# Performance work log

Measured on AMD Instinct MI355X. Metric: run time of the kernel, lower is better.

Reference implementation:

```python
import jax, jax.numpy as jnp
import numpy as np

N_NODES = 50000
IN_CH = 256
OUT_CH = 128
HID = 2 * OUT_CH  # 256
N_EDGES = 800000


def setup_inputs() -> dict:
    key = jax.random.key(0)
    ks = jax.random.split(key, 12)
    glorot = lambda k, shape: jax.random.normal(k, shape, jnp.float32) * (2.0 / sum(shape)) ** 0.5
    return {
        "x": jax.random.normal(ks[0], (N_NODES, IN_CH), jnp.float32),
        "edge_index": jax.random.randint(ks[1], (2, N_EDGES), 0, N_NODES),
        "conv_w": glorot(ks[2], (IN_CH, HID)),      # MetaGCNConv weight: x @ W
        "conv_b": jnp.zeros((HID,), jnp.float32),
        "fc1_w": glorot(ks[3], (HID, HID)), "fc1_b": jnp.zeros((HID,), jnp.float32),
        "fc2_w": glorot(ks[4], (HID, HID)), "fc2_b": jnp.zeros((HID,), jnp.float32),
        "fc3_w": glorot(ks[5], (OUT_CH, HID)), "fc3_b": jnp.zeros((OUT_CH,), jnp.float32),
        "fc4_w": glorot(ks[6], (OUT_CH, HID)), "fc4_b": jnp.zeros((OUT_CH,), jnp.float32),
    }


def reference(x, edge_index, conv_w, conv_b, fc1_w, fc1_b, fc2_w, fc2_b, fc3_w, fc3_b, fc4_w, fc4_b):
    N = x.shape[0]
    # GCN with added self-loops and symmetric normalization (PyG GCNConv semantics)
    loop = jnp.arange(N)
    src = jnp.concatenate([edge_index[0], loop])
    dst = jnp.concatenate([edge_index[1], loop])
    xw = x @ conv_w  # [N, HID]
    ones = jnp.ones_like(src, dtype=x.dtype)
    deg = jax.ops.segment_sum(ones, src, num_segments=N)
    dinv = jnp.where(deg > 0, jax.lax.rsqrt(deg), 0.0)
    norm = dinv[src] * dinv[dst]  # [E+N]
    agg = jax.ops.segment_sum(norm[:, None] * xw[src], dst, num_segments=N)  # [N, HID]
    h = jax.nn.relu(agg + conv_b)
    s = h.sum(0)  # [HID]
    lin = lambda v, w, b: jnp.tanh(v @ w.T + b)
    return (lin(s, fc1_w, fc1_b), lin(s, fc2_w, fc2_b), lin(s, fc3_w, fc3_b), lin(s, fc4_w, fc4_b))
```

## Files before the change

kernel.cpp:

```cpp
#include <hip/hip_runtime.h>
#include <math.h>

#define CH 256
#define BCAP 64

typedef short bf16x8 __attribute__((ext_vector_type(8)));
typedef float f32x4 __attribute__((ext_vector_type(4)));
typedef unsigned int u32;

__device__ __forceinline__ unsigned short f2bf(float f) {
    u32 u = __float_as_uint(f);
    u += 0x7FFFu + ((u >> 16) & 1u);
    return (unsigned short)(u >> 16);
}
__device__ __forceinline__ float bf2f(unsigned short h) {
    return __uint_as_float(((u32)h) << 16);
}
__device__ __forceinline__ float lo16f(u32 q) { return __uint_as_float(q << 16); }
__device__ __forceinline__ float hi16f(u32 q) { return __uint_as_float(q & 0xffff0000u); }
__device__ __forceinline__ u32 pkbf(float a, float b) {
    u32 ua = __float_as_uint(a) + 0x8000u;
    u32 ub = __float_as_uint(b) + 0x8000u;
    return __builtin_amdgcn_perm(ub, ua, 0x07060302u);
}
__device__ __forceinline__ void async16(const void* g, void* l) {
    __builtin_amdgcn_global_load_lds((const __attribute__((address_space(1))) u32*)g,
                                     (__attribute__((address_space(3))) u32*)l, 16, 0, 0);
}

__global__ __launch_bounds__(256) void prep_kernel(const float* __restrict__ W,
                                                   unsigned short* __restrict__ whiT,
                                                   unsigned short* __restrict__ wloT,
                                                   float4* __restrict__ zbase,
                                                   int zcount4) {
    int b = blockIdx.x, t = threadIdx.x;
    if (b < 64) {
#pragma unroll
        for (int i = 0; i < 4; i++) {
            int n = b * 4 + i;
            float w = W[(size_t)t * CH + n];
            unsigned short hi = f2bf(w);
            unsigned short lo = f2bf(w - bf2f(hi));
            whiT[(size_t)n * CH + t] = hi;
            wloT[(size_t)n * CH + t] = lo;
        }
    } else {
        int i = (b - 64) * 256 + t;
        int stride = 104 * 256;
        float4 z = make_float4(0.f, 0.f, 0.f, 0.f);
        for (; i < zcount4; i += stride) zbase[i] = z;
    }
}

__global__ __launch_bounds__(256) void mega_kernel(const float* __restrict__ x,
                                                   const unsigned short* __restrict__ whiT,
                                                   const unsigned short* __restrict__ wloT,
                                                   const int* __restrict__ ei,
                                                   unsigned* __restrict__ cnt_src,
                                                   unsigned* __restrict__ cnt_dst,
                                                   unsigned* __restrict__ col,
                                                   unsigned short* __restrict__ y,
                                                   int M, int E, int G) {
    int b = blockIdx.x, t = threadIdx.x;
    if (b < 2 * G && !(b & 1)) {
        __shared__ __align__(16) unsigned short smA [128 * 32];
        __shared__ __align__(16) unsigned short smBh[128 * 32];
        __shared__ __align__(16) unsigned short smBl[128 * 32];
        int g = b >> 1;
        int lane = t & 63, w = t >> 6;
        int m0 = (g >> 1) * 128;
        int n0 = (g & 1) * 128;
        int mo = (w >> 1) * 64, no = (w & 1) * 64;
        int quad = lane >> 4, l16 = lane & 15;

        f32x4 acc[4][4] = {};

        int arow = t >> 1, ahalf = t & 1;
        int gm = min(m0 + arow, M - 1);
        const float* xrow = x + (size_t)gm * CH + ahalf * 16;
        int idx0 = t, idx1 = t + 256;
        size_t gb0 = (size_t)(n0 + (idx0 >> 2)) * CH + (idx0 & 3) * 8;
        size_t gb1 = (size_t)(n0 + (idx1 >> 2)) * CH + (idx1 & 3) * 8;

        for (int k0 = 0; k0 < CH; k0 += 32) {
            const float4* xp = (const float4*)(xrow + k0);
            float4 v0 = xp[0], v1 = xp[1], v2 = xp[2], v3 = xp[3];
            async16(&whiT[gb0 + k0], &smBh[idx0 * 8]);
            async16(&whiT[gb1 + k0], &smBh[idx1 * 8]);
            async16(&wloT[gb0 + k0], &smBl[idx0 * 8]);
            async16(&wloT[gb1 + k0], &smBl[idx1 * 8]);
            uint4 w0 = make_uint4(pkbf(v0.x, v0.y), pkbf(v0.z, v0.w),
                                  pkbf(v1.x, v1.y), pkbf(v1.z, v1.w));
            uint4 w1 = make_uint4(pkbf(v2.x, v2.y), pkbf(v2.z, v2.w),
                                  pkbf(v3.x, v3.y), pkbf(v3.z, v3.w));
            *(uint4*)&smA[arow * 32 + ahalf * 16]     = w0;
            *(uint4*)&smA[arow * 32 + ahalf * 16 + 8] = w1;
            __syncthreads();

            bf16x8 a[4], bh[4], bl[4];
#pragma unroll
            for (int i = 0; i < 4; i++)
                a[i] = *(const bf16x8*)&smA[(mo + i * 16 + l16) * 32 + quad * 8];
#pragma unroll
            for (int j = 0; j < 4; j++) {
                bh[j] = *(const bf16x8*)&smBh[(no + j * 16 + l16) * 32 + quad * 8];
                bl[j] = *(const bf16x8*)&smBl[(no + j * 16 + l16) * 32 + quad * 8];
            }
#pragma unroll
            for (int i = 0; i < 4; i++)
#pragma unroll
                for (int j = 0; j < 4; j++) {
                    acc[i][j] = __builtin_amdgcn_mfma_f32_16x16x32_bf16(a[i], bh[j], acc[i][j], 0, 0, 0);
                    acc[i][j] = __builtin_amdgcn_mfma_f32_16x16x32_bf16(a[i], bl[j], acc[i][j], 0, 0, 0);
                }
            __syncthreads();
        }
#pragma unroll
        for (int i = 0; i < 4; i++) {
            int mbase = m0 + mo + i * 16 + quad * 4;
#pragma unroll
            for (int r = 0; r < 4; r++) {
                int m = mbase + r;
                if (m < M) {
#pragma unroll
                    for (int j = 0; j < 4; j++) {
                        int ncol = n0 + no + j * 16 + l16;
                        int s = ncol >> 5, c = ncol & 31;
                        y[((size_t)s * M + m) * 32 + c] = f2bf(acc[i][j][r]);
                    }
                }
            }
        }
    } else {
        int fb = (b < 2 * G) ? (b >> 1) : (b - G);
        if (fb >= 1024) return;
        int i = fb * 256 + t;
        int stride = 1024 * 256;
        for (; i < E; i += stride) {
            int s = ei[i];
            int d = ei[E + i];
            atomicAdd(&cnt_src[s], 1u);
            unsigned pos = atomicAdd(&cnt_dst[d], 1u);
            if (pos < BCAP) col[(size_t)d * BCAP + pos] = (unsigned)s;
        }
    }
}

__global__ __launch_bounds__(256) void scale_kernel(unsigned short* __restrict__ y,
                                                    const unsigned* __restrict__ cnt_src,
                                                    int M) {
    int gid = blockIdx.x * 256 + threadIdx.x;
    int gstride = gridDim.x * 256;
    int total4 = M * 4;
    uint4* yq = (uint4*)y;
    for (int s = 0; s < 8; s++) {
        for (int c = gid; c < total4; c += gstride) {
            int m = c >> 2;
            float dv = rsqrtf((float)(cnt_src[m] + 1u));
            uint4 q = yq[(size_t)s * total4 + c];
            q.x = pkbf(dv * lo16f(q.x), dv * hi16f(q.x));
            q.y = pkbf(dv * lo16f(q.y), dv * hi16f(q.y));
            q.z = pkbf(dv * lo16f(q.z), dv * hi16f(q.z));
            q.w = pkbf(dv * lo16f(q.w), dv * hi16f(q.w));
            yq[(size_t)s * total4 + c] = q;
        }
    }
}

__global__ __launch_bounds__(256) void gather_kernel(const unsigned short* __restrict__ y,
                                                     const unsigned* __restrict__ cnt_src,
                                                     const unsigned* __restrict__ cnt_dst,
                                                     const unsigned* __restrict__ col,
                                                     const float* __restrict__ bias,
                                                     float* __restrict__ s_sum, int N) {
    int t = threadIdx.x;
    int lane = t & 63, wv = t >> 6;
    int slice = blockIdx.x & 7;
    int grp   = blockIdx.x >> 3;
    int ng = lane >> 4;
    int g  = (lane >> 2) & 3;
    int li = lane & 3;
    const unsigned short* ys = y + (size_t)slice * N * 32;

    float b8[8];
#pragma unroll
    for (int j = 0; j < 8; j++) b8[j] = bias[slice * 32 + li * 8 + j];

    float ts[8] = {0.f, 0.f, 0.f, 0.f, 0.f, 0.f, 0.f, 0.f};

    int wid = grp * 4 + wv;
    int nw  = (gridDim.x >> 3) * 4;

    for (int base = wid * 4; base < N; base += nw * 4) {
        int n = min(base + ng, N - 1);
        unsigned deg = min(cnt_dst[n], (unsigned)BCAP);
        unsigned cnt = deg + 1;
        float gnm = (g == 0 && base + ng < N) ? 1.f : 0.f;
        unsigned mc = cnt;
        mc = max(mc, (unsigned)__shfl_xor((int)mc, 16, 64));
        mc = max(mc, (unsigned)__shfl_xor((int)mc, 32, 64));

        const unsigned* cb = col + (size_t)n * BCAP;
        float acc[8] = {0.f, 0.f, 0.f, 0.f, 0.f, 0.f, 0.f, 0.f};
        for (unsigned k = 0; k < mc; k += 4) {
            unsigned r = k + g;
            unsigned src = (r < deg) ? cb[r] : (unsigned)n;
            float m = (r < cnt) ? 1.f : 0.f;
            uint4 q = *(const uint4*)(ys + (size_t)src * 32 + li * 8);
            acc[0] = fmaf(m, lo16f(q.x), acc[0]);
            acc[1] = fmaf(m, hi16f(q.x), acc[1]);
            acc[2] = fmaf(m, lo16f(q.y), acc[2]);
            acc[3] = fmaf(m, hi16f(q.y), acc[3]);
            acc[4] = fmaf(m, lo16f(q.z), acc[4]);
            acc[5] = fmaf(m, hi16f(q.z), acc[5]);
            acc[6] = fmaf(m, lo16f(q.w), acc[6]);
            acc[7] = fmaf(m, hi16f(q.w), acc[7]);
        }
        float dv = rsqrtf((float)(cnt_src[n] + 1u));
#pragma unroll
        for (int j = 0; j < 8; j++) {
            float v = acc[j];
            v += __shfl_xor(v, 4, 64);
            v += __shfl_xor(v, 8, 64);
            float h = fmaxf(fmaf(dv, v, b8[j]), 0.f);
            ts[j] = fmaf(gnm, h, ts[j]);
        }
    }

#pragma unroll
    for (int j = 0; j < 8; j++) {
        float v = ts[j];
        v += __shfl_xor(v, 16, 64);
        v += __shfl_xor(v, 32, 64);
        ts[j] = v;
    }

    __shared__ float red[4][32];
    if (lane < 4) {
#pragma unroll
        for (int j = 0; j < 8; j++) red[wv][lane * 8 + j] = ts[j];
    }
    __syncthreads();
    if (t < 32) {
        atomicAdd(&s_sum[slice * 32 + t],
                  red[0][t] + red[1][t] + red[2][t] + red[3][t]);
    }
}

__global__ __launch_bounds__(256) void fc_kernel(const float* __restrict__ s_sum,
                                                 const float* __restrict__ fc1_w, const float* __restrict__ fc1_b,
                                                 const float* __restrict__ fc2_w, const float* __restrict__ fc2_b,
                                                 const float* __restrict__ fc3_w, const float* __restrict__ fc3_b,
                                                 const float* __restrict__ fc4_w, const float* __restrict__ fc4_b,
                                                 float* __restrict__ out) {
    int wid  = (blockIdx.x * blockDim.x + threadIdx.x) >> 6;
    int lane = threadIdx.x & 63;
    if (wid >= 768) return;
    const float* w; const float* b; int row, obase;
    if (wid < 256)      { w = fc1_w; b = fc1_b; row = wid;       obase = 0;   }
    else if (wid < 512) { w = fc2_w; b = fc2_b; row = wid - 256; obase = 256; }
    else if (wid < 640) { w = fc3_w; b = fc3_b; row = wid - 512; obase = 512; }
    else                { w = fc4_w; b = fc4_b; row = wid - 640; obase = 640; }
    float4 wv = *(const float4*)&w[(size_t)row * 256 + lane * 4];
    float4 sv = *(const float4*)&s_sum[lane * 4];
    float d = wv.x * sv.x + wv.y * sv.y + wv.z * sv.z + wv.w * sv.w;
#pragma unroll
    for (int off = 32; off; off >>= 1) d += __shfl_down(d, off, 64);
    if (lane == 0) out[obase + row] = tanhf(d + b[row]);
}

extern "C" void kernel_launch(void* const* d_in, const int* in_sizes, int n_in,
                              void* d_out, int out_size, void* d_ws, size_t ws_size,
                              hipStream_t stream) {
    const float* x      = (const float*)d_in[0];
    const int*   ei     = (const int*)d_in[1];
    const float* conv_w = (const float*)d_in[2];
    const float* conv_b = (const float*)d_in[3];
    const float* fc1_w  = (const float*)d_in[4];
    const float* fc1_b  = (const float*)d_in[5];
    const float* fc2_w  = (const float*)d_in[6];
    const float* fc2_b  = (const float*)d_in[7];
    const float* fc3_w  = (const float*)d_in[8];
    const float* fc3_b  = (const float*)d_in[9];
    const float* fc4_w  = (const float*)d_in[10];
    const float* fc4_b  = (const float*)d_in[11];
    float* out = (float*)d_out;

    const int N = in_sizes[0] / CH;
    const int E = in_sizes[1] / 2;
    const int G = ((N + 127) / 128) * 2;

    char* ws = (char*)d_ws;
    size_t off = 0;
    auto alloc = [&](size_t bytes) -> void* {
        off = (off + 255) & ~(size_t)255;
        void* p = ws + off;
        off += bytes;
        return p;
    };
    unsigned* cnt_src = (unsigned*)alloc((size_t)N * 4);
    unsigned* cnt_dst = (unsigned*)alloc((size_t)N * 4);
    float*    s_sum   = (float*)alloc((size_t)CH * 4);
    size_t zero_bytes = off;
    unsigned* col     = (unsigned*)alloc((size_t)N * BCAP * 4);
    unsigned short* whiT = (unsigned short*)alloc((size_t)CH * CH * 2);
    unsigned short* wloT = (unsigned short*)alloc((size_t)CH * CH * 2);
    unsigned short* y    = (unsigned short*)alloc((size_t)N * CH * 2);

    int zcount4 = (int)((zero_bytes + 15) / 16);

    prep_kernel<<<168, 256, 0, stream>>>(conv_w, whiT, wloT, (float4*)ws, zcount4);
    mega_kernel<<<G + 1024, 256, 0, stream>>>(x, whiT, wloT, ei,
                                              cnt_src, cnt_dst, col, y, N, E, G);
    scale_kernel<<<1024, 256, 0, stream>>>(y, cnt_src, N);
    gather_kernel<<<2048, 256, 0, stream>>>(y, cnt_src, cnt_dst, col, conv_b, s_sum, N);
    fc_kernel<<<192, 256, 0, stream>>>(s_sum,
                                       fc1_w, fc1_b, fc2_w, fc2_b,
                                       fc3_w, fc3_b, fc4_w, fc4_b, out);
}
```

Baseline: 243.9 us.

## Compute source degrees in prep kernel and fuse dinv scaling into GEMM epilogue

```diff
diff --git a/kernel.cpp b/kernel.cpp
--- a/kernel.cpp
+++ b/kernel.cpp
@@ -31,8 +31,10 @@
 __global__ __launch_bounds__(256) void prep_kernel(const float* __restrict__ W,
                                                    unsigned short* __restrict__ whiT,
                                                    unsigned short* __restrict__ wloT,
+                                                   const int* __restrict__ ei,
+                                                   unsigned* __restrict__ cnt_src,
                                                    float4* __restrict__ zbase,
-                                                   int zcount4) {
+                                                   int zcount4, int E) {
     int b = blockIdx.x, t = threadIdx.x;
     if (b < 64) {
 #pragma unroll
@@ -44,11 +46,15 @@
             whiT[(size_t)n * CH + t] = hi;
             wloT[(size_t)n * CH + t] = lo;
         }
-    } else {
+    } else if (b < 128) {
         int i = (b - 64) * 256 + t;
-        int stride = 104 * 256;
+        int stride = 64 * 256;
         float4 z = make_float4(0.f, 0.f, 0.f, 0.f);
         for (; i < zcount4; i += stride) zbase[i] = z;
+    } else {
+        int i = (b - 128) * 256 + t;
+        int stride = 512 * 256;
+        for (; i < E; i += stride) atomicAdd(&cnt_src[ei[i]], 1u);
     }
 }
 
@@ -56,7 +62,7 @@
                                                    const unsigned short* __restrict__ whiT,
                                                    const unsigned short* __restrict__ wloT,
                                                    const int* __restrict__ ei,
-                                                   unsigned* __restrict__ cnt_src,
+                                                   const unsigned* __restrict__ cnt_src,
                                                    unsigned* __restrict__ cnt_dst,
                                                    unsigned* __restrict__ col,
                                                    unsigned short* __restrict__ y,
@@ -122,11 +128,12 @@
             for (int r = 0; r < 4; r++) {
                 int m = mbase + r;
                 if (m < M) {
+                    float dv = rsqrtf((float)(cnt_src[m] + 1u));
 #pragma unroll
                     for (int j = 0; j < 4; j++) {
                         int ncol = n0 + no + j * 16 + l16;
                         int s = ncol >> 5, c = ncol & 31;
-                        y[((size_t)s * M + m) * 32 + c] = f2bf(acc[i][j][r]);
+                        y[((size_t)s * M + m) * 32 + c] = f2bf(dv * acc[i][j][r]);
                     }
                 }
             }
@@ -139,30 +146,8 @@
         for (; i < E; i += stride) {
             int s = ei[i];
             int d = ei[E + i];
-            atomicAdd(&cnt_src[s], 1u);
             unsigned pos = atomicAdd(&cnt_dst[d], 1u);
             if (pos < BCAP) col[(size_t)d * BCAP + pos] = (unsigned)s;
-        }
-    }
-}
-
-__global__ __launch_bounds__(256) void scale_kernel(unsigned short* __restrict__ y,
-                                                    const unsigned* __restrict__ cnt_src,
-                                                    int M) {
-    int gid = blockIdx.x * 256 + threadIdx.x;
-    int gstride = gridDim.x * 256;
-    int total4 = M * 4;
-    uint4* yq = (uint4*)y;
-    for (int s = 0; s < 8; s++) {
-        for (int c = gid; c < total4; c += gstride) {
-            int m = c >> 2;
-            float dv = rsqrtf((float)(cnt_src[m] + 1u));
-            uint4 q = yq[(size_t)s * total4 + c];
-            q.x = pkbf(dv * lo16f(q.x), dv * hi16f(q.x));
-            q.y = pkbf(dv * lo16f(q.y), dv * hi16f(q.y));
-            q.z = pkbf(dv * lo16f(q.z), dv * hi16f(q.z));
-            q.w = pkbf(dv * lo16f(q.w), dv * hi16f(q.w));
-            yq[(size_t)s * total4 + c] = q;
         }
     }
 }
@@ -216,13 +201,13 @@
             acc[6] = fmaf(m, lo16f(q.w), acc[6]);
             acc[7] = fmaf(m, hi16f(q.w), acc[7]);
         }
-        float dv = rsqrtf((float)(cnt_src[n] + 1u));
+        float dvn = rsqrtf((float)(cnt_src[n] + 1u));
 #pragma unroll
         for (int j = 0; j < 8; j++) {
             float v = acc[j];
             v += __shfl_xor(v, 4, 64);
             v += __shfl_xor(v, 8, 64);
-            float h = fmaxf(fmaf(dv, v, b8[j]), 0.f);
+            float h = fmaxf(fmaf(dvn, v, b8[j]), 0.f);
             ts[j] = fmaf(gnm, h, ts[j]);
         }
     }
@@ -299,20 +284,22 @@
         return p;
     };
     unsigned* cnt_src = (unsigned*)alloc((size_t)N * 4);
+    size_t z0 = off;
     unsigned* cnt_dst = (unsigned*)alloc((size_t)N * 4);
     float*    s_sum   = (float*)alloc((size_t)CH * 4);
-    size_t zero_bytes = off;
+    size_t zbytes = off - z0;
     unsigned* col     = (unsigned*)alloc((size_t)N * BCAP * 4);
     unsigned short* whiT = (unsigned short*)alloc((size_t)CH * CH * 2);
     unsigned short* wloT = (unsigned short*)alloc((size_t)CH * CH * 2);
     unsigned short* y    = (unsigned short*)alloc((size_t)N * CH * 2);
 
-    int zcount4 = (int)((zero_bytes + 15) / 16);
-
-    prep_kernel<<<168, 256, 0, stream>>>(conv_w, whiT, wloT, (float4*)ws, zcount4);
+    int zcount4 = (int)((zbytes + 15) / 16);
+
+    hipMemsetAsync(cnt_src, 0, (size_t)N * 4, stream);
+    prep_kernel<<<640, 256, 0, stream>>>(conv_w, whiT, wloT, ei, cnt_src,
+                                         (float4*)(ws + z0), zcount4, E);
     mega_kernel<<<G + 1024, 256, 0, stream>>>(x, whiT, wloT, ei,
                                               cnt_src, cnt_dst, col, y, N, E, G);
-    scale_kernel<<<1024, 256, 0, stream>>>(y, cnt_src, N);
     gather_kernel<<<2048, 256, 0, stream>>>(y, cnt_src, cnt_dst, col, conv_b, s_sum, N);
     fc_kernel<<<192, 256, 0, stream>>>(s_sum,
                                        fc1_w, fc1_b, fc2_w, fc2_b,
```

New measurement: 262.1 us. 7.5% more time.
